# Kernel tuning notes

Hardware: AMD Instinct MI355X
Metric: run time of the kernel (lower is better)

The kernel has to match this reference:

```python
import jax, jax.numpy as jnp
import numpy as np

N_NODES = 50000
N_EDGES = 800000
F_IN = 128
HID = 64
N_LAYERS = 3
N_GRAPHS = 64
N_CLASS = 2


def setup_inputs() -> dict:
    key = jax.random.key(0)
    ks = jax.random.split(key, 8)
    x = jax.random.normal(ks[0], (N_NODES, F_IN), jnp.float32)
    edge_index = jax.random.randint(ks[1], (2, N_EDGES), 0, N_NODES, dtype=jnp.int32)
    # sorted, balanced graph assignment so every graph id appears (max-pool safe)
    batch = (jnp.arange(N_NODES, dtype=jnp.int32) * N_GRAPHS) // N_NODES

    def lin(k, fi, fo):
        return jax.random.normal(k, (fi, fo), jnp.float32) / np.sqrt(fi).astype(np.float32)

    W1 = lin(ks[2], F_IN, HID)
    W2 = lin(ks[3], HID, HID)
    W3 = lin(ks[4], HID, HID)
    lin1_W = lin(ks[5], 3 * N_LAYERS * HID, HID)
    lin2_W = lin(ks[6], HID, N_CLASS)
    return dict(
        x=x,
        W1=W1, b1=jnp.zeros((HID,), jnp.float32),
        W2=W2, b2=jnp.zeros((HID,), jnp.float32),
        W3=W3, b3=jnp.zeros((HID,), jnp.float32),
        lin1_W=lin1_W, lin1_b=jnp.zeros((HID,), jnp.float32),
        lin2_W=lin2_W, lin2_b=jnp.zeros((N_CLASS,), jnp.float32),
        edge_index=edge_index, batch=batch,
    )


def reference(x, W1, b1, W2, b2, W3, b3, lin1_W, lin1_b, lin2_W, lin2_b,
              edge_index, batch):
    src, dst = edge_index[0], edge_index[1]
    # GCN symmetric normalization with self-loops (computed once, shared by layers)
    deg = jax.ops.segment_sum(jnp.ones((N_EDGES,), jnp.float32), dst, N_NODES) + 1.0
    dinv = jax.lax.rsqrt(deg)                      # [N]
    enorm = dinv[src] * dinv[dst]                  # [E]
    self_norm = (dinv * dinv)[:, None]             # [N,1] self-loop coeff

    def gcn_conv(h, W, b):
        h = h @ W                                  # [N, HID]
        agg = jax.ops.segment_sum(h[src] * enorm[:, None], dst, N_NODES)
        return agg + self_norm * h + b

    h = jax.nn.relu(gcn_conv(x, W1, b1))
    xs = [h]
    for W, b in ((W2, b2), (W3, b3)):
        h = jax.nn.relu(gcn_conv(h, W, b))
        xs.append(h)
    hcat = jnp.concatenate(xs, axis=1)             # JK 'cat': [N, 3*HID]

    add = jax.ops.segment_sum(hcat, batch, N_GRAPHS)
    cnt = jax.ops.segment_sum(jnp.ones((N_NODES,), jnp.float32), batch, N_GRAPHS)
    mean = add / cnt[:, None]
    mx = jax.ops.segment_max(hcat, batch, N_GRAPHS)
    g = jnp.concatenate([add, mean, mx], axis=1)   # [G, 9*HID]

    g = jax.nn.relu(g @ lin1_W + lin1_b)
    # dropout p=0.5 is identity in eval mode
    logits = g @ lin2_W + lin2_b
    return jax.nn.log_softmax(logits, axis=-1)
```

## Files before the change

### kernel.cpp

```cpp
#include <hip/hip_runtime.h>
#include <hip/hip_fp16.h>

#define N_NODES 50000
#define N_EDGES 800000
#define F_IN 128
#define HID 64
#define N_GRAPHS 64

#define SCAN_B ((N_NODES + 255) / 256)
#define FUSE_B ((N_EDGES + 255) / 256)

typedef _Float16 half8 __attribute__((ext_vector_type(8)));
typedef float f32x4 __attribute__((ext_vector_type(4)));

__global__ void deg_pack(const int* __restrict__ ei, int* __restrict__ ideg,
                         unsigned short* __restrict__ rank, int* __restrict__ pcnt, int E,
                         const float* __restrict__ W1, const float* __restrict__ W2,
                         const float* __restrict__ W3,
                         __half* __restrict__ W1t, __half* __restrict__ W2t,
                         __half* __restrict__ W3t) {
    int i = blockIdx.x * blockDim.x + threadIdx.x;
    if (i * 4 < E) {
        int4 d = ((const int4*)(ei + E))[i];
        unsigned short r0 = (unsigned short)atomicAdd(&ideg[d.x], 1);
        unsigned short r1 = (unsigned short)atomicAdd(&ideg[d.y], 1);
        unsigned short r2 = (unsigned short)atomicAdd(&ideg[d.z], 1);
        unsigned short r3 = (unsigned short)atomicAdd(&ideg[d.w], 1);
        ushort4 rr; rr.x = r0; rr.y = r1; rr.z = r2; rr.w = r3;
        *(ushort4*)(rank + i * 4) = rr;
    }
    if (i < 64) pcnt[i] = 0;
    if (i < 8192) {
        int f = i >> 7, k = i & 127;
        W1t[i] = __float2half(W1[k * 64 + f]);
    } else if (i < 12288) {
        int j = i - 8192;
        int f = j >> 6, k = j & 63;
        W2t[j] = __float2half(W2[k * 64 + f]);
    } else if (i < 16384) {
        int l = i - 12288;
        int f = l >> 6, k = l & 63;
        W3t[l] = __float2half(W3[k * 64 + f]);
    }
}

__global__ void scan_part(const int* __restrict__ ideg, int* __restrict__ bsum,
                          const int* __restrict__ batch,
                          float* __restrict__ padd, unsigned int* __restrict__ pmax,
                          int* __restrict__ pcnt, int n) {
    __shared__ int s[256];
    __shared__ int hcnt[N_GRAPHS];
    int t = threadIdx.x;
    if (blockIdx.x < 48) {
        int z = blockIdx.x * 256 + t;
        padd[z] = 0.f;
        pmax[z] = 0u;
    }
    if (t < N_GRAPHS) hcnt[t] = 0;
    int i = blockIdx.x * 256 + t;
    s[t] = (i < n) ? ideg[i] : 0;
    __syncthreads();
    if (i < n) atomicAdd(&hcnt[batch[i]], 1);
    for (int o = 128; o > 0; o >>= 1) {
        if (t < o) s[t] += s[t + o];
        __syncthreads();
    }
    if (t == 0) bsum[blockIdx.x] = s[0];
    if (t < N_GRAPHS && hcnt[t]) atomicAdd(&pcnt[t], hcnt[t]);
}

__global__ void scan_final(const int* __restrict__ ideg, const int* __restrict__ bsum,
                           int* __restrict__ offs, float* __restrict__ dinv, int n) {
    __shared__ int s[256];
    __shared__ int sb[256];
    int t = threadIdx.x;
    int i = blockIdx.x * 256 + t;
    int v = (i < n) ? ideg[i] : 0;
    s[t] = v;
    sb[t] = (t < SCAN_B) ? bsum[t] : 0;
    __syncthreads();
    for (int o = 1; o < 256; o <<= 1) {
        int u  = (t >= o) ? s[t - o] : 0;
        int ub = (t >= o) ? sb[t - o] : 0;
        __syncthreads();
        s[t] += u; sb[t] += ub;
        __syncthreads();
    }
    int base = (blockIdx.x == 0) ? 0 : sb[blockIdx.x - 1];
    int excl = base + s[t] - v;
    if (i < n) {
        offs[i] = excl;
        dinv[i] = rsqrtf((float)v + 1.0f);
    }
    if (i == n - 1) offs[n] = excl + v;
}

__global__ __launch_bounds__(256) void fused_fill_mm1(
        const int* __restrict__ ei, const float* __restrict__ dinv,
        const int* __restrict__ offs, const unsigned short* __restrict__ rank,
        unsigned short* __restrict__ csr,
        const float* __restrict__ X, const __half* __restrict__ W1t,
        __half* __restrict__ Y16, int E) {
    constexpr int SX = 136;
    __shared__ __half sXh[16 * SX];
    int tid = threadIdx.x;

    int e = blockIdx.x * 256 + tid;
    unsigned short srcu = (unsigned short)(ei[e] & 0xFFFF);
    int d = ei[E + e];
    int pos = offs[d] + (int)rank[e];

    int lane = tid & 63;
    int r = lane & 15, h = lane >> 4;
    int w = tid >> 6;
    const half8* Brow = (const half8*)(W1t + (size_t)(w * 16 + r) * F_IN + h * 8);
    half8 b0 = Brow[0];
    half8 b1 = Brow[4];
    half8 b2 = Brow[8];
    half8 b3 = Brow[12];

    int nodeBase = blockIdx.x * 16;
#pragma unroll
    for (int p = tid; p < 512; p += 256) {
        int row = p >> 5, c4 = p & 31;
        float4 v = *(const float4*)(X + (size_t)(nodeBase + row) * F_IN + c4 * 4);
        __half2 ab = __floats2half2_rn(v.x, v.y);
        __half2 cd = __floats2half2_rn(v.z, v.w);
        uint2 u; u.x = *(unsigned int*)&ab; u.y = *(unsigned int*)&cd;
        *(uint2*)&sXh[row * SX + c4 * 4] = u;
    }
    __syncthreads();

    f32x4 acc = {0.f, 0.f, 0.f, 0.f};
    half8 a0 = *(const half8*)&sXh[r * SX +  0 + h * 8];
    half8 a1 = *(const half8*)&sXh[r * SX + 32 + h * 8];
    half8 a2 = *(const half8*)&sXh[r * SX + 64 + h * 8];
    half8 a3 = *(const half8*)&sXh[r * SX + 96 + h * 8];
    acc = __builtin_amdgcn_mfma_f32_16x16x32_f16(a0, b0, acc, 0, 0, 0);
    acc = __builtin_amdgcn_mfma_f32_16x16x32_f16(a1, b1, acc, 0, 0, 0);
    acc = __builtin_amdgcn_mfma_f32_16x16x32_f16(a2, b2, acc, 0, 0, 0);
    acc = __builtin_amdgcn_mfma_f32_16x16x32_f16(a3, b3, acc, 0, 0, 0);
    int nodeT = nodeBase + h * 4;
    float4 dv = *(const float4*)(dinv + nodeT);
    acc[0] *= dv.x; acc[1] *= dv.y; acc[2] *= dv.z; acc[3] *= dv.w;
#pragma unroll
    for (int reg = 0; reg < 4; ++reg)
        Y16[(size_t)(nodeT + reg) * 64 + w * 16 + r] = __float2half(acc[reg]);

    csr[pos] = srcu;
}

__global__ __launch_bounds__(256) void matmul64_h(
        const __half* __restrict__ X, const __half* __restrict__ Wt,
        const float* __restrict__ dinv, __half* __restrict__ Y16, int n) {
    int tid = threadIdx.x;
    int nodeBase = blockIdx.x * 64;
    int lane = tid & 63;
    int r = lane & 15, h = lane >> 4;
    int w = tid >> 6;
    int rowA = nodeBase + w * 16 + r;
    const half8* Arow = (const half8*)(X + (size_t)rowA * 64 + h * 8);
    half8 a0 = Arow[0];
    half8 a1 = Arow[4];
    int nodeT = nodeBase + w * 16 + h * 4;
    float4 dv = *(const float4*)(dinv + nodeT);
#pragma unroll
    for (int ft = 0; ft < 4; ++ft) {
        const half8* Brow = (const half8*)(Wt + (size_t)(ft * 16 + r) * 64 + h * 8);
        half8 b0 = Brow[0];
        half8 b1 = Brow[4];
        f32x4 acc = {0.f, 0.f, 0.f, 0.f};
        acc = __builtin_amdgcn_mfma_f32_16x16x32_f16(a0, b0, acc, 0, 0, 0);
        acc = __builtin_amdgcn_mfma_f32_16x16x32_f16(a1, b1, acc, 0, 0, 0);
        acc[0] *= dv.x; acc[1] *= dv.y; acc[2] *= dv.z; acc[3] *= dv.w;
#pragma unroll
        for (int reg = 0; reg < 4; ++reg) {
            int node = nodeT + reg;
            if (node < n) Y16[(size_t)node * 64 + ft * 16 + r] = __float2half(acc[reg]);
        }
    }
}

__global__ void agg_kernel(const __half* __restrict__ hp16, const float* __restrict__ dinv,
                           const int* __restrict__ offs, const unsigned short* __restrict__ csr,
                           const float* __restrict__ b, __half* __restrict__ hout, int n) {
    int node = blockIdx.x * 4 + (threadIdx.x >> 6);
    if (node >= n) return;
    int lane = threadIdx.x & 63;
    int g = lane >> 3;
    int sub = lane & 7;
    int beg = offs[node], end = offs[node + 1];

    float dn = dinv[node];
    uint4 sv = *(const uint4*)(hp16 + (size_t)node * 64 + sub * 8);
    float4 bA = *(const float4*)(b + sub * 8);
    float4 bB = *(const float4*)(b + sub * 8 + 4);

    float a0 = 0.f, a1 = 0.f, a2 = 0.f, a3 = 0.f;
    float a4 = 0.f, a5 = 0.f, a6 = 0.f, a7 = 0.f;
    int lim = end - 1;
#pragma unroll 1
    for (int base0 = beg; base0 < end; base0 += 32) {
        int base = base0 + g * 4;
        if (base < end) {
            int i0 = base, i1 = min(base + 1, lim), i2 = min(base + 2, lim), i3 = min(base + 3, lim);
            unsigned short s0 = csr[i0], s1 = csr[i1], s2 = csr[i2], s3 = csr[i3];
            uint4 hv0 = *(const uint4*)(hp16 + (size_t)s0 * 64 + sub * 8);
            uint4 hv1 = *(const uint4*)(hp16 + (size_t)s1 * 64 + sub * 8);
            uint4 hv2 = *(const uint4*)(hp16 + (size_t)s2 * 64 + sub * 8);
            uint4 hv3 = *(const uint4*)(hp16 + (size_t)s3 * 64 + sub * 8);
#pragma unroll
            for (int j = 0; j < 4; ++j) {
                uint4 hvj = (j == 0) ? hv0 : (j == 1) ? hv1 : (j == 2) ? hv2 : hv3;
                float w = (base + j < end) ? 1.f : 0.f;
                float2 f01 = __half22float2(*(const __half2*)&hvj.x);
                float2 f23 = __half22float2(*(const __half2*)&hvj.y);
                float2 f45 = __half22float2(*(const __half2*)&hvj.z);
                float2 f67 = __half22float2(*(const __half2*)&hvj.w);
                a0 += f01.x * w; a1 += f01.y * w; a2 += f23.x * w; a3 += f23.y * w;
                a4 += f45.x * w; a5 += f45.y * w; a6 += f67.x * w; a7 += f67.y * w;
            }
        }
    }
#pragma unroll
    for (int m = 8; m <= 32; m <<= 1) {
        a0 += __shfl_xor(a0, m); a1 += __shfl_xor(a1, m);
        a2 += __shfl_xor(a2, m); a3 += __shfl_xor(a3, m);
        a4 += __shfl_xor(a4, m); a5 += __shfl_xor(a5, m);
        a6 += __shfl_xor(a6, m); a7 += __shfl_xor(a7, m);
    }

    float2 s01 = __half22float2(*(const __half2*)&sv.x);
    float2 s23 = __half22float2(*(const __half2*)&sv.y);
    float2 s45 = __half22float2(*(const __half2*)&sv.z);
    float2 s67 = __half22float2(*(const __half2*)&sv.w);
    float4 rA, rB;
    rA.x = dn * (a0 + s01.x) + bA.x;  rA.x = rA.x > 0.f ? rA.x : 0.f;
    rA.y = dn * (a1 + s01.y) + bA.y;  rA.y = rA.y > 0.f ? rA.y : 0.f;
    rA.z = dn * (a2 + s23.x) + bA.z;  rA.z = rA.z > 0.f ? rA.z : 0.f;
    rA.w = dn * (a3 + s23.y) + bA.w;  rA.w = rA.w > 0.f ? rA.w : 0.f;
    rB.x = dn * (a4 + s45.x) + bB.x;  rB.x = rB.x > 0.f ? rB.x : 0.f;
    rB.y = dn * (a5 + s45.y) + bB.y;  rB.y = rB.y > 0.f ? rB.y : 0.f;
    rB.z = dn * (a6 + s67.x) + bB.z;  rB.z = rB.z > 0.f ? rB.z : 0.f;
    rB.w = dn * (a7 + s67.y) + bB.w;  rB.w = rB.w > 0.f ? rB.w : 0.f;
    if (g == 0) {
        __half2 p0 = __floats2half2_rn(rA.x, rA.y);
        __half2 p1 = __floats2half2_rn(rA.z, rA.w);
        __half2 p2 = __floats2half2_rn(rB.x, rB.y);
        __half2 p3 = __floats2half2_rn(rB.z, rB.w);
        uint4 st;
        st.x = *(unsigned int*)&p0; st.y = *(unsigned int*)&p1;
        st.z = *(unsigned int*)&p2; st.w = *(unsigned int*)&p3;
        *(uint4*)(hout + (size_t)node * 64 + sub * 8) = st;
    }
}

__global__ __launch_bounds__(192) void pool_kernel(
        const __half* __restrict__ h1, const __half* __restrict__ h2,
        const __half* __restrict__ h3, const int* __restrict__ batch,
        float* __restrict__ padd, unsigned int* __restrict__ pmax, int n, int chunk) {
    __shared__ float lsum[8][192];
    __shared__ float lmax[8][192];
    int t = threadIdx.x;
    int stream = t / 24;
    int oct = t % 24;
    int L = oct >> 3, sub = oct & 7;
    int f0 = L * 64 + sub * 8;
    const __half* src = (L == 0) ? h1 : (L == 1) ? h2 : h3;
    int start = blockIdx.x * chunk;
    int end = min(start + chunk, n);
    if (start >= end) return;
    int gtail = batch[end - 1];

    float s[8] = {0.f,0.f,0.f,0.f,0.f,0.f,0.f,0.f};
    float m[8] = {0.f,0.f,0.f,0.f,0.f,0.f,0.f,0.f};
    int node = start + stream;
    int gcur = (node < end) ? batch[node] : gtail;
    for (; node < end; node += 8) {
        int bg = batch[node];
        if (bg != gcur) {
#pragma unroll
            for (int j = 0; j < 8; ++j) {
                unsafeAtomicAdd(&padd[gcur * 192 + f0 + j], s[j]);
                atomicMax(&pmax[gcur * 192 + f0 + j], __float_as_uint(m[j]));
                s[j] = 0.f; m[j] = 0.f;
            }
            gcur = bg;
        }
        uint4 hv = *(const uint4*)(src + (size_t)node * 64 + sub * 8);
        const __half2* hp = (const __half2*)&hv;
#pragma unroll
        for (int q = 0; q < 4; ++q) {
            float2 f2 = __half22float2(hp[q]);
            s[2*q]   += f2.x;  m[2*q]   = fmaxf(m[2*q],   f2.x);
            s[2*q+1] += f2.y;  m[2*q+1] = fmaxf(m[2*q+1], f2.y);
        }
    }
    if (gcur != gtail) {
#pragma unroll
        for (int j = 0; j < 8; ++j) {
            unsafeAtomicAdd(&padd[gcur * 192 + f0 + j], s[j]);
            atomicMax(&pmax[gcur * 192 + f0 + j], __float_as_uint(m[j]));
            s[j] = 0.f; m[j] = 0.f;
        }
    }
#pragma unroll
    for (int j = 0; j < 8; ++j) {
        lsum[stream][f0 + j] = s[j];
        lmax[stream][f0 + j] = m[j];
    }
    __syncthreads();
    float ts = 0.f, tm = 0.f;
#pragma unroll
    for (int st = 0; st < 8; ++st) {
        ts += lsum[st][t];
        tm = fmaxf(tm, lmax[st][t]);
    }
    unsafeAtomicAdd(&padd[gtail * 192 + t], ts);
    atomicMax(&pmax[gtail * 192 + t], __float_as_uint(tm));
}

__global__ void mlp_kernel(const float* __restrict__ padd, const unsigned int* __restrict__ pmax,
                           const int* __restrict__ pcnt,
                           const float* __restrict__ lin1_W, const float* __restrict__ lin1_b,
                           const float* __restrict__ lin2_W, const float* __restrict__ lin2_b,
                           float* __restrict__ out) {
    int g = blockIdx.x;
    int t = threadIdx.x;
    __shared__ float gv[576];
    __shared__ float hid[64];
    float cnt = (float)pcnt[g];
    for (int i = t; i < 192; i += 64) {
        float a = padd[g * 192 + i];
        gv[i] = a;
        gv[192 + i] = a / cnt;
        gv[384 + i] = __uint_as_float(pmax[g * 192 + i]);
    }
    __syncthreads();
    float acc = lin1_b[t];
#pragma unroll 8
    for (int k = 0; k < 576; ++k) acc += gv[k] * lin1_W[k * 64 + t];
    hid[t] = acc > 0.0f ? acc : 0.0f;
    __syncthreads();
    if (t == 0) {
        float l0 = lin2_b[0], l1 = lin2_b[1];
        for (int k = 0; k < 64; ++k) {
            l0 += hid[k] * lin2_W[k * 2 + 0];
            l1 += hid[k] * lin2_W[k * 2 + 1];
        }
        float m = fmaxf(l0, l1);
        float lse = m + logf(expf(l0 - m) + expf(l1 - m));
        out[g * 2 + 0] = l0 - lse;
        out[g * 2 + 1] = l1 - lse;
    }
}

extern "C" void kernel_launch(void* const* d_in, const int* in_sizes, int n_in,
                              void* d_out, int out_size, void* d_ws, size_t ws_size,
                              hipStream_t stream) {
    const float* x      = (const float*)d_in[0];
    const float* W1     = (const float*)d_in[1];
    const float* b1     = (const float*)d_in[2];
    const float* W2     = (const float*)d_in[3];
    const float* b2     = (const float*)d_in[4];
    const float* W3     = (const float*)d_in[5];
    const float* b3     = (const float*)d_in[6];
    const float* lin1_W = (const float*)d_in[7];
    const float* lin1_b = (const float*)d_in[8];
    const float* lin2_W = (const float*)d_in[9];
    const float* lin2_b = (const float*)d_in[10];
    const int*   ei     = (const int*)d_in[11];
    const int*   batch  = (const int*)d_in[12];
    float* out = (float*)d_out;

    char* ws = (char*)d_ws;
    size_t off = 0;
    auto alloc = [&](size_t bytes) {
        void* p = ws + off;
        off = (off + bytes + 255) & ~(size_t)255;
        return p;
    };
    int*   ideg    = (int*)  alloc(N_NODES * 4);
    float* dinv    = (float*)alloc(N_NODES * 4);
    int*   offs    = (int*)  alloc((N_NODES + 1) * 4);
    int*   bsum    = (int*)  alloc(SCAN_B * 4);
    unsigned short* rank = (unsigned short*)alloc((size_t)N_EDGES * 2);
    unsigned short* csr  = (unsigned short*)alloc((size_t)N_EDGES * 2);
    __half* P      = (__half*)alloc((size_t)N_NODES * 64 * 2);
    __half* h1     = (__half*)alloc((size_t)N_NODES * 64 * 2);
    __half* h2     = (__half*)alloc((size_t)N_NODES * 64 * 2);
    __half* h3     = (__half*)alloc((size_t)N_NODES * 64 * 2);
    __half* W1t    = (__half*)alloc(64 * 128 * 2);
    __half* W2t    = (__half*)alloc(64 * 64 * 2);
    __half* W3t    = (__half*)alloc(64 * 64 * 2);
    float* padd    = (float*)alloc(N_GRAPHS * 192 * 4);
    unsigned int* pmax = (unsigned int*)alloc(N_GRAPHS * 192 * 4);
    int*   pcnt    = (int*) alloc(N_GRAPHS * 4);

    hipMemsetAsync(ideg, 0, N_NODES * 4, stream);
    deg_pack<<<(N_EDGES / 4 + 255) / 256, 256, 0, stream>>>(ei, ideg, rank, pcnt, N_EDGES,
                                                            W1, W2, W3, W1t, W2t, W3t);
    scan_part <<<SCAN_B, 256, 0, stream>>>(ideg, bsum, batch, padd, pmax, pcnt, N_NODES);
    scan_final<<<SCAN_B, 256, 0, stream>>>(ideg, bsum, offs, dinv, N_NODES);

    const int mmGrid  = (N_NODES + 63) / 64;
    const int aggGrid = (N_NODES + 3) / 4;

    fused_fill_mm1<<<FUSE_B, 256, 0, stream>>>(ei, dinv, offs, rank, csr, x, W1t, P, N_EDGES);
    agg_kernel<<<aggGrid, 256, 0, stream>>>(P, dinv, offs, csr, b1, h1, N_NODES);
    matmul64_h<<<mmGrid, 256, 0, stream>>>(h1, W2t, dinv, P, N_NODES);
    agg_kernel<<<aggGrid, 256, 0, stream>>>(P, dinv, offs, csr, b2, h2, N_NODES);
    matmul64_h<<<mmGrid, 256, 0, stream>>>(h2, W3t, dinv, P, N_NODES);
    agg_kernel<<<aggGrid, 256, 0, stream>>>(P, dinv, offs, csr, b3, h3, N_NODES);

    const int chunk = (N_NODES + 511) / 512;
    pool_kernel<<<512, 192, 0, stream>>>(h1, h2, h3, batch, padd, pmax, N_NODES, chunk);
    mlp_kernel<<<N_GRAPHS, 64, 0, stream>>>(padd, pmax, pcnt, lin1_W, lin1_b, lin2_W, lin2_b, out);
}
```

Measured before the change: 281.0 us.

## Replace prefix-scan CSR with fixed-slot adjacency plus overflow list

Builds the adjacency as fixed 32-slot segments per destination node, with ranks packed as bytes. Edges past slot 32 go to a global overflow list that every aggregation thread scans. This removes both scan kernels and the dinv/offs arrays, and inverse-sqrt degrees are now recomputed inline from ideg. One memset zeroes the degree, pool and overflow buffers together. The trade-off is a larger padded CSR and a per-node loop over the overflow list. Edges are dropped if overflow exceeds its capacity, which skewed graphs could hit.

Result: no change. 285.9 us (+1.7%).

```diff
diff --git a/kernel.cpp b/kernel.cpp
--- a/kernel.cpp
+++ b/kernel.cpp
@@ -6,30 +6,39 @@
 #define F_IN 128
 #define HID 64
 #define N_GRAPHS 64
-
-#define SCAN_B ((N_NODES + 255) / 256)
+#define SEG 32
+#define OVF_CAP 4096
+
 #define FUSE_B ((N_EDGES + 255) / 256)
 
 typedef _Float16 half8 __attribute__((ext_vector_type(8)));
 typedef float f32x4 __attribute__((ext_vector_type(4)));
 
 __global__ void deg_pack(const int* __restrict__ ei, int* __restrict__ ideg,
-                         unsigned short* __restrict__ rank, int* __restrict__ pcnt, int E,
+                         unsigned char* __restrict__ rank, const int* __restrict__ batch,
+                         int* __restrict__ pcnt, int E,
                          const float* __restrict__ W1, const float* __restrict__ W2,
                          const float* __restrict__ W3,
                          __half* __restrict__ W1t, __half* __restrict__ W2t,
                          __half* __restrict__ W3t) {
-    int i = blockIdx.x * blockDim.x + threadIdx.x;
+    __shared__ int hcnt[N_GRAPHS];
+    int t = threadIdx.x;
+    if (t < N_GRAPHS) hcnt[t] = 0;
+    __syncthreads();
+    int i = blockIdx.x * blockDim.x + t;
     if (i * 4 < E) {
         int4 d = ((const int4*)(ei + E))[i];
-        unsigned short r0 = (unsigned short)atomicAdd(&ideg[d.x], 1);
-        unsigned short r1 = (unsigned short)atomicAdd(&ideg[d.y], 1);
-        unsigned short r2 = (unsigned short)atomicAdd(&ideg[d.z], 1);
-        unsigned short r3 = (unsigned short)atomicAdd(&ideg[d.w], 1);
-        ushort4 rr; rr.x = r0; rr.y = r1; rr.z = r2; rr.w = r3;
-        *(ushort4*)(rank + i * 4) = rr;
-    }
-    if (i < 64) pcnt[i] = 0;
+        int r0 = atomicAdd(&ideg[d.x], 1);
+        int r1 = atomicAdd(&ideg[d.y], 1);
+        int r2 = atomicAdd(&ideg[d.z], 1);
+        int r3 = atomicAdd(&ideg[d.w], 1);
+        unsigned int packed = (unsigned int)min(r0, 255)
+                            | ((unsigned int)min(r1, 255) << 8)
+                            | ((unsigned int)min(r2, 255) << 16)
+                            | ((unsigned int)min(r3, 255) << 24);
+        *(unsigned int*)(rank + i * 4) = packed;
+    }
+    if (i < N_NODES) atomicAdd(&hcnt[batch[i]], 1);
     if (i < 8192) {
         int f = i >> 7, k = i & 127;
         W1t[i] = __float2half(W1[k * 64 + f]);
@@ -42,63 +51,14 @@
         int f = l >> 6, k = l & 63;
         W3t[l] = __float2half(W3[k * 64 + f]);
     }
-}
-
-__global__ void scan_part(const int* __restrict__ ideg, int* __restrict__ bsum,
-                          const int* __restrict__ batch,
-                          float* __restrict__ padd, unsigned int* __restrict__ pmax,
-                          int* __restrict__ pcnt, int n) {
-    __shared__ int s[256];
-    __shared__ int hcnt[N_GRAPHS];
-    int t = threadIdx.x;
-    if (blockIdx.x < 48) {
-        int z = blockIdx.x * 256 + t;
-        padd[z] = 0.f;
-        pmax[z] = 0u;
-    }
-    if (t < N_GRAPHS) hcnt[t] = 0;
-    int i = blockIdx.x * 256 + t;
-    s[t] = (i < n) ? ideg[i] : 0;
-    __syncthreads();
-    if (i < n) atomicAdd(&hcnt[batch[i]], 1);
-    for (int o = 128; o > 0; o >>= 1) {
-        if (t < o) s[t] += s[t + o];
-        __syncthreads();
-    }
-    if (t == 0) bsum[blockIdx.x] = s[0];
+    __syncthreads();
     if (t < N_GRAPHS && hcnt[t]) atomicAdd(&pcnt[t], hcnt[t]);
 }
 
-__global__ void scan_final(const int* __restrict__ ideg, const int* __restrict__ bsum,
-                           int* __restrict__ offs, float* __restrict__ dinv, int n) {
-    __shared__ int s[256];
-    __shared__ int sb[256];
-    int t = threadIdx.x;
-    int i = blockIdx.x * 256 + t;
-    int v = (i < n) ? ideg[i] : 0;
-    s[t] = v;
-    sb[t] = (t < SCAN_B) ? bsum[t] : 0;
-    __syncthreads();
-    for (int o = 1; o < 256; o <<= 1) {
-        int u  = (t >= o) ? s[t - o] : 0;
-        int ub = (t >= o) ? sb[t - o] : 0;
-        __syncthreads();
-        s[t] += u; sb[t] += ub;
-        __syncthreads();
-    }
-    int base = (blockIdx.x == 0) ? 0 : sb[blockIdx.x - 1];
-    int excl = base + s[t] - v;
-    if (i < n) {
-        offs[i] = excl;
-        dinv[i] = rsqrtf((float)v + 1.0f);
-    }
-    if (i == n - 1) offs[n] = excl + v;
-}
-
 __global__ __launch_bounds__(256) void fused_fill_mm1(
-        const int* __restrict__ ei, const float* __restrict__ dinv,
-        const int* __restrict__ offs, const unsigned short* __restrict__ rank,
-        unsigned short* __restrict__ csr,
+        const int* __restrict__ ei, const int* __restrict__ ideg,
+        const unsigned char* __restrict__ rank, unsigned short* __restrict__ csr,
+        unsigned int* __restrict__ ovf, int* __restrict__ ovfCnt,
         const float* __restrict__ X, const __half* __restrict__ W1t,
         __half* __restrict__ Y16, int E) {
     constexpr int SX = 136;
@@ -108,7 +68,8 @@
     int e = blockIdx.x * 256 + tid;
     unsigned short srcu = (unsigned short)(ei[e] & 0xFFFF);
     int d = ei[E + e];
-    int pos = offs[d] + (int)rank[e];
+    int rk = rank[e];
+    int pos = (rk < SEG) ? (d * SEG + rk) : -1;
 
     int lane = tid & 63;
     int r = lane & 15, h = lane >> 4;
@@ -141,18 +102,26 @@
     acc = __builtin_amdgcn_mfma_f32_16x16x32_f16(a2, b2, acc, 0, 0, 0);
     acc = __builtin_amdgcn_mfma_f32_16x16x32_f16(a3, b3, acc, 0, 0, 0);
     int nodeT = nodeBase + h * 4;
-    float4 dv = *(const float4*)(dinv + nodeT);
-    acc[0] *= dv.x; acc[1] *= dv.y; acc[2] *= dv.z; acc[3] *= dv.w;
+    int4 dg = *(const int4*)(ideg + nodeT);
+    acc[0] *= rsqrtf((float)dg.x + 1.0f);
+    acc[1] *= rsqrtf((float)dg.y + 1.0f);
+    acc[2] *= rsqrtf((float)dg.z + 1.0f);
+    acc[3] *= rsqrtf((float)dg.w + 1.0f);
 #pragma unroll
     for (int reg = 0; reg < 4; ++reg)
         Y16[(size_t)(nodeT + reg) * 64 + w * 16 + r] = __float2half(acc[reg]);
 
-    csr[pos] = srcu;
+    if (pos >= 0) {
+        csr[pos] = srcu;
+    } else {
+        int ix = atomicAdd(ovfCnt, 1);
+        if (ix < OVF_CAP) ovf[ix] = ((unsigned int)d << 16) | (unsigned int)srcu;
+    }
 }
 
 __global__ __launch_bounds__(256) void matmul64_h(
         const __half* __restrict__ X, const __half* __restrict__ Wt,
-        const float* __restrict__ dinv, __half* __restrict__ Y16, int n) {
+        const int* __restrict__ ideg, __half* __restrict__ Y16, int n) {
     int tid = threadIdx.x;
     int nodeBase = blockIdx.x * 64;
     int lane = tid & 63;
@@ -163,7 +132,12 @@
     half8 a0 = Arow[0];
     half8 a1 = Arow[4];
     int nodeT = nodeBase + w * 16 + h * 4;
-    float4 dv = *(const float4*)(dinv + nodeT);
+    int4 dg = *(const int4*)(ideg + nodeT);
+    float4 dv;
+    dv.x = rsqrtf((float)dg.x + 1.0f);
+    dv.y = rsqrtf((float)dg.y + 1.0f);
+    dv.z = rsqrtf((float)dg.z + 1.0f);
+    dv.w = rsqrtf((float)dg.w + 1.0f);
 #pragma unroll
     for (int ft = 0; ft < 4; ++ft) {
         const half8* Brow = (const half8*)(Wt + (size_t)(ft * 16 + r) * 64 + h * 8);
@@ -181,45 +155,59 @@
     }
 }
 
-__global__ void agg_kernel(const __half* __restrict__ hp16, const float* __restrict__ dinv,
-                           const int* __restrict__ offs, const unsigned short* __restrict__ csr,
-                           const float* __restrict__ b, __half* __restrict__ hout, int n) {
+__global__ void agg_kernel(const __half* __restrict__ hp16, const int* __restrict__ ideg,
+                           const unsigned short* __restrict__ csr, const float* __restrict__ b,
+                           const unsigned int* __restrict__ ovf, const int* __restrict__ ovfCnt,
+                           __half* __restrict__ hout, int n) {
     int node = blockIdx.x * 4 + (threadIdx.x >> 6);
     if (node >= n) return;
     int lane = threadIdx.x & 63;
     int g = lane >> 3;
     int sub = lane & 7;
-    int beg = offs[node], end = offs[node + 1];
-
-    float dn = dinv[node];
+    int deg = ideg[node];
+    int beg = node * SEG;
+    int end = beg + min(deg, SEG);
+    float dn = rsqrtf((float)deg + 1.0f);
+
     uint4 sv = *(const uint4*)(hp16 + (size_t)node * 64 + sub * 8);
     float4 bA = *(const float4*)(b + sub * 8);
     float4 bB = *(const float4*)(b + sub * 8 + 4);
 
     float a0 = 0.f, a1 = 0.f, a2 = 0.f, a3 = 0.f;
     float a4 = 0.f, a5 = 0.f, a6 = 0.f, a7 = 0.f;
-    int lim = end - 1;
-#pragma unroll 1
-    for (int base0 = beg; base0 < end; base0 += 32) {
-        int base = base0 + g * 4;
-        if (base < end) {
-            int i0 = base, i1 = min(base + 1, lim), i2 = min(base + 2, lim), i3 = min(base + 3, lim);
-            unsigned short s0 = csr[i0], s1 = csr[i1], s2 = csr[i2], s3 = csr[i3];
-            uint4 hv0 = *(const uint4*)(hp16 + (size_t)s0 * 64 + sub * 8);
-            uint4 hv1 = *(const uint4*)(hp16 + (size_t)s1 * 64 + sub * 8);
-            uint4 hv2 = *(const uint4*)(hp16 + (size_t)s2 * 64 + sub * 8);
-            uint4 hv3 = *(const uint4*)(hp16 + (size_t)s3 * 64 + sub * 8);
-#pragma unroll
-            for (int j = 0; j < 4; ++j) {
-                uint4 hvj = (j == 0) ? hv0 : (j == 1) ? hv1 : (j == 2) ? hv2 : hv3;
-                float w = (base + j < end) ? 1.f : 0.f;
-                float2 f01 = __half22float2(*(const __half2*)&hvj.x);
-                float2 f23 = __half22float2(*(const __half2*)&hvj.y);
-                float2 f45 = __half22float2(*(const __half2*)&hvj.z);
-                float2 f67 = __half22float2(*(const __half2*)&hvj.w);
-                a0 += f01.x * w; a1 += f01.y * w; a2 += f23.x * w; a3 += f23.y * w;
-                a4 += f45.x * w; a5 += f45.y * w; a6 += f67.x * w; a7 += f67.y * w;
-            }
+    int base = beg + g * 4;
+    if (base < end) {
+        int lim = end - 1;
+        int i1 = min(base + 1, lim), i2 = min(base + 2, lim), i3 = min(base + 3, lim);
+        unsigned short s0 = csr[base], s1 = csr[i1], s2 = csr[i2], s3 = csr[i3];
+        uint4 hv0 = *(const uint4*)(hp16 + (size_t)s0 * 64 + sub * 8);
+        uint4 hv1 = *(const uint4*)(hp16 + (size_t)s1 * 64 + sub * 8);
+        uint4 hv2 = *(const uint4*)(hp16 + (size_t)s2 * 64 + sub * 8);
+        uint4 hv3 = *(const uint4*)(hp16 + (size_t)s3 * 64 + sub * 8);
+#pragma unroll
+        for (int j = 0; j < 4; ++j) {
+            uint4 hvj = (j == 0) ? hv0 : (j == 1) ? hv1 : (j == 2) ? hv2 : hv3;
+            float w = (base + j < end) ? 1.f : 0.f;
+            float2 f01 = __half22float2(*(const __half2*)&hvj.x);
+            float2 f23 = __half22float2(*(const __half2*)&hvj.y);
+            float2 f45 = __half22float2(*(const __half2*)&hvj.z);
+            float2 f67 = __half22float2(*(const __half2*)&hvj.w);
+            a0 += f01.x * w; a1 += f01.y * w; a2 += f23.x * w; a3 += f23.y * w;
+            a4 += f45.x * w; a5 += f45.y * w; a6 += f67.x * w; a7 += f67.y * w;
+        }
+    }
+    int on = min(*ovfCnt, OVF_CAP);
+    for (int k = 0; k < on; ++k) {
+        unsigned int pe = ovf[k];
+        if ((int)(pe >> 16) == node && g == (k & 7)) {
+            int ss = (int)(pe & 0xFFFFu);
+            uint4 hv = *(const uint4*)(hp16 + (size_t)ss * 64 + sub * 8);
+            float2 f01 = __half22float2(*(const __half2*)&hv.x);
+            float2 f23 = __half22float2(*(const __half2*)&hv.y);
+            float2 f45 = __half22float2(*(const __half2*)&hv.z);
+            float2 f67 = __half22float2(*(const __half2*)&hv.w);
+            a0 += f01.x; a1 += f01.y; a2 += f23.x; a3 += f23.y;
+            a4 += f45.x; a5 += f45.y; a6 += f67.x; a7 += f67.y;
         }
     }
 #pragma unroll
@@ -381,11 +369,14 @@
         return p;
     };
     int*   ideg    = (int*)  alloc(N_NODES * 4);
-    float* dinv    = (float*)alloc(N_NODES * 4);
-    int*   offs    = (int*)  alloc((N_NODES + 1) * 4);
-    int*   bsum    = (int*)  alloc(SCAN_B * 4);
-    unsigned short* rank = (unsigned short*)alloc((size_t)N_EDGES * 2);
-    unsigned short* csr  = (unsigned short*)alloc((size_t)N_EDGES * 2);
+    int*   pcnt    = (int*)  alloc(N_GRAPHS * 4);
+    float* padd    = (float*)alloc(N_GRAPHS * 192 * 4);
+    unsigned int* pmax = (unsigned int*)alloc(N_GRAPHS * 192 * 4);
+    int*   ovfCnt  = (int*)  alloc(256);
+    size_t zeroBytes = off;
+    unsigned char*  rank = (unsigned char*)alloc((size_t)N_EDGES);
+    unsigned short* csr  = (unsigned short*)alloc((size_t)N_NODES * SEG * 2);
+    unsigned int*   ovf  = (unsigned int*)alloc(OVF_CAP * 4);
     __half* P      = (__half*)alloc((size_t)N_NODES * 64 * 2);
     __half* h1     = (__half*)alloc((size_t)N_NODES * 64 * 2);
     __half* h2     = (__half*)alloc((size_t)N_NODES * 64 * 2);
@@ -393,25 +384,21 @@
     __half* W1t    = (__half*)alloc(64 * 128 * 2);
     __half* W2t    = (__half*)alloc(64 * 64 * 2);
     __half* W3t    = (__half*)alloc(64 * 64 * 2);
-    float* padd    = (float*)alloc(N_GRAPHS * 192 * 4);
-    unsigned int* pmax = (unsigned int*)alloc(N_GRAPHS * 192 * 4);
-    int*   pcnt    = (int*) alloc(N_GRAPHS * 4);
-
-    hipMemsetAsync(ideg, 0, N_NODES * 4, stream);
-    deg_pack<<<(N_EDGES / 4 + 255) / 256, 256, 0, stream>>>(ei, ideg, rank, pcnt, N_EDGES,
-                                                            W1, W2, W3, W1t, W2t, W3t);
-    scan_part <<<SCAN_B, 256, 0, stream>>>(ideg, bsum, batch, padd, pmax, pcnt, N_NODES);
-    scan_final<<<SCAN_B, 256, 0, stream>>>(ideg, bsum, offs, dinv, N_NODES);
+
+    hipMemsetAsync(ws, 0, zeroBytes, stream);
+    deg_pack<<<(N_EDGES / 4 + 255) / 256, 256, 0, stream>>>(ei, ideg, rank, batch, pcnt,
+                                                            N_EDGES, W1, W2, W3, W1t, W2t, W3t);
 
     const int mmGrid  = (N_NODES + 63) / 64;
     const int aggGrid = (N_NODES + 3) / 4;
 
-    fused_fill_mm1<<<FUSE_B, 256, 0, stream>>>(ei, dinv, offs, rank, csr, x, W1t, P, N_EDGES);
-    agg_kernel<<<aggGrid, 256, 0, stream>>>(P, dinv, offs, csr, b1, h1, N_NODES);
-    matmul64_h<<<mmGrid, 256, 0, stream>>>(h1, W2t, dinv, P, N_NODES);
-    agg_kernel<<<aggGrid, 256, 0, stream>>>(P, dinv, offs, csr, b2, h2, N_NODES);
-    matmul64_h<<<mmGrid, 256, 0, stream>>>(h2, W3t, dinv, P, N_NODES);
-    agg_kernel<<<aggGrid, 256, 0, stream>>>(P, dinv, offs, csr, b3, h3, N_NODES);
+    fused_fill_mm1<<<FUSE_B, 256, 0, stream>>>(ei, ideg, rank, csr, ovf, ovfCnt,
+                                               x, W1t, P, N_EDGES);
+    agg_kernel<<<aggGrid, 256, 0, stream>>>(P, ideg, csr, b1, ovf, ovfCnt, h1, N_NODES);
+    matmul64_h<<<mmGrid, 256, 0, stream>>>(h1, W2t, ideg, P, N_NODES);
+    agg_kernel<<<aggGrid, 256, 0, stream>>>(P, ideg, csr, b2, ovf, ovfCnt, h2, N_NODES);
+    matmul64_h<<<mmGrid, 256, 0, stream>>>(h2, W3t, ideg, P, N_NODES);
+    agg_kernel<<<aggGrid, 256, 0, stream>>>(P, ideg, csr, b3, ovf, ovfCnt, h3, N_NODES);
 
     const int chunk = (N_NODES + 511) / 512;
     pool_kernel<<<512, 192, 0, stream>>>(h1, h2, h3, batch, padd, pmax, N_NODES, chunk);
```
